# Kernel optimization log

Hardware: AMD Instinct MI355X
Metric: run time of the kernel (lower is better)

## Reference

```python
import jax, jax.numpy as jnp
import numpy as np

B, T, C = 4, 2048, 1024
NH, HS = 16, 64            # n_head, head_size
BL, SL = 32, 16            # block_length, stride_length


def setup_inputs() -> dict:
    key = jax.random.key(0)
    ks = jax.random.split(key, 7)
    def lin(k, shape, fan_in):
        return jax.random.normal(k, shape, jnp.float32) * (1.0 / np.sqrt(fan_in))
    return {
        "x": jax.random.normal(ks[0], (B, T, C), jnp.float32),
        "W_attn": lin(ks[1], (3 * C, C), C),          # c_attn weight (bias=False)
        "W_proj": lin(ks[2], (C, C), C),              # c_proj weight
        "pos_emb": jax.random.normal(ks[3], (T, HS), jnp.float32) * 0.02,
        "W_fc": lin(ks[4], (4 * HS, BL * HS), BL * HS),   # compression c_fc
        "W_cproj": lin(ks[5], (HS, 4 * HS), 4 * HS),      # compression c_proj
        "ln_w": jnp.ones((HS,), jnp.float32),             # compression LayerNorm (bias=False)
    }


def _compress(h, pos_emb, W_fc, W_cproj, ln_w):
    # h: [B, nh, T, hs] -> [B, nh, num_blocks, hs] ; sliding windows of len BL, stride SL
    Bb, nh, Tt, hs = h.shape
    nb = max(1, (Tt - BL) // SL + 1)
    idx = jnp.arange(nb)[:, None] * SL + jnp.arange(BL)[None, :]        # [nb, BL]
    blocks = h[:, :, idx, :] + pos_emb[:BL][None, None, None, :, :]     # [B,nh,nb,BL,hs]
    flat = blocks.reshape(Bb, nh, nb, BL * hs)
    z = jax.nn.gelu(jnp.einsum('bnkf,gf->bnkg', flat, W_fc), approximate=False)
    z = jnp.einsum('bnkg,hg->bnkh', z, W_cproj)
    mu = jnp.mean(z, axis=-1, keepdims=True)
    var = jnp.var(z, axis=-1, keepdims=True)
    return (z - mu) / jnp.sqrt(var + 1e-5) * ln_w


def reference(x, W_attn, W_proj, pos_emb, W_fc, W_cproj, ln_w):
    Bb, Tt, Cc = x.shape
    qkv = x @ W_attn.T                                   # [B,T,3C]
    q, k, v = jnp.split(qkv, 3, axis=-1)
    q = q.reshape(Bb, Tt, NH, HS).transpose(0, 2, 1, 3)  # [B,nh,T,hs]
    k = k.reshape(Bb, Tt, NH, HS).transpose(0, 2, 1, 3)
    v = v.reshape(Bb, Tt, NH, HS).transpose(0, 2, 1, 3)

    # Computed (and discarded) exactly as in the torch forward.
    _kc = _compress(k, pos_emb, W_fc, W_cproj, ln_w)
    _vc = _compress(v, pos_emb, W_fc, W_cproj, ln_w)

    # Flash branch: is_causal=True -> attn_mask=None -> plain causal SDPA
    scale = 1.0 / np.sqrt(HS)
    scores = jnp.einsum('bhqd,bhkd->bhqk', q, k) * scale          # [B,nh,T,T]
    causal = jnp.tril(jnp.ones((Tt, Tt), dtype=bool))
    scores = jnp.where(causal, scores, -jnp.inf)
    att = jax.nn.softmax(scores, axis=-1)
    y = jnp.einsum('bhqk,bhkd->bhqd', att, v)                     # [B,nh,T,hs]
    y = y.transpose(0, 2, 1, 3).reshape(Bb, Tt, Cc)
    return y @ W_proj.T
```

## Files before the change

kernel.cpp:

```cpp
#include <hip/hip_runtime.h>
#include <hip/hip_bf16.h>
#include <stdint.h>


typedef __bf16 bf16x8 __attribute__((ext_vector_type(8)));
typedef float f32x4 __attribute__((ext_vector_type(4)));
typedef __hip_bfloat16 bf16;

#define B_ 4
#define T_ 2048
#define C_ 1024
#define NH_ 16
#define HS_ 64
#define NEG_BIG (-30000.0f)
#define SCALE_LOG2E 0.180336880111f

__device__ __forceinline__ bool detect_fp32(const unsigned short* px) {
  const int lane = threadIdx.x & 63;
  const unsigned short u = px[2 * lane];
  const int e = (u >> 7) & 0xff;
  const bool plausible = (e >= 117) && (e <= 137);
  return __popcll(__ballot(plausible)) < 32;
}

__device__ __forceinline__ void load_lds16(const bf16* g, bf16* l) {
  __builtin_amdgcn_global_load_lds(
      (const __attribute__((address_space(1))) void*)(uintptr_t)g,
      (__attribute__((address_space(3))) void*)(uintptr_t)l, 16, 0, 0);
}

__device__ __forceinline__ uint4 ld8f(const void* base, size_t elt) {
  const float* fp = (const float*)base + elt;
  float4 f0 = *(const float4*)(fp);
  float4 f1 = *(const float4*)(fp + 4);
  union { bf16 h[8]; uint4 u; } r;
  r.h[0] = __float2bfloat16(f0.x); r.h[1] = __float2bfloat16(f0.y);
  r.h[2] = __float2bfloat16(f0.z); r.h[3] = __float2bfloat16(f0.w);
  r.h[4] = __float2bfloat16(f1.x); r.h[5] = __float2bfloat16(f1.y);
  r.h[6] = __float2bfloat16(f1.z); r.h[7] = __float2bfloat16(f1.w);
  return r.u;
}

__global__ __launch_bounds__(256) void convert3(
    const void* __restrict__ x, const void* __restrict__ wa,
    const void* __restrict__ wp, bf16* __restrict__ xb, bf16* __restrict__ wab,
    bf16* __restrict__ wpb, const unsigned short* __restrict__ probe) {
  const bool f32 = detect_fp32(probe);
  int blk = blockIdx.x;
  const void* src;
  bf16* dst;
  if (blk < 4096) {
    src = x; dst = xb;
  } else if (blk < 4096 + 1536) {
    blk -= 4096; src = wa; dst = wab;
  } else {
    blk -= 4096 + 1536; src = wp; dst = wpb;
  }
  const size_t i = ((size_t)blk * 256 + threadIdx.x) * 8;
  if (f32)
    *(uint4*)(dst + i) = ld8f(src, i);
  else
    *(uint4*)(dst + i) = *(const uint4*)((const bf16*)src + i);
}

template <int IN_MODE, int OUT_MODE>
__global__ __launch_bounds__(256, 2) void gemm_bt(
    const void* __restrict__ A, const void* __restrict__ B, void* __restrict__ C,
    bf16* __restrict__ k_ws, bf16* __restrict__ v_ws,
    const unsigned short* __restrict__ in_probe,
    const unsigned short* __restrict__ out_probe, int M, int N, int K) {
  __shared__ bf16 As[2][128 * 32];
  __shared__ bf16 Bs[2][128 * 32];

  const bool f32b = in_probe ? detect_fp32(in_probe) : false;
  const bool f32a = (IN_MODE == 0) && f32b;
  const bool f32out =
      (OUT_MODE == 0) && (out_probe ? detect_fp32(out_probe) : false);

  const int tid = threadIdx.x;
  const int lane = tid & 63;
  const int wid = tid >> 6;
  const int quad = lane >> 4;
  const int col = lane & 15;
  const int m0 = blockIdx.y * 128;
  const int n0 = blockIdx.x * 128;
  const int wm = (wid >> 1) * 64;
  const int wn = (wid & 1) * 64;
  const bool vsec = (OUT_MODE == 1) && ((n0 >> 10) == 2);

  const size_t arow = (size_t)(m0 + (tid >> 2));
  const size_t brow = (size_t)(n0 + (tid >> 2));
  const int chunk = (tid & 3) * 8;
  const size_t astep = (IN_MODE == 0) ? (size_t)64 * K : (size_t)64 * HS_;

  f32x4 acc[4][4] = {};

  auto a_ptr = [&](int k0) -> const bf16* {
    if (IN_MODE == 0) return (const bf16*)A + arow * K + chunk + k0;
    const int b = m0 >> 11;
    const int tloc = (m0 & 2047) + (tid >> 2);
    return (const bf16*)A +
           ((((size_t)b * NH_) + (k0 >> 6)) * T_ + tloc) * HS_ + (k0 & 32) +
           chunk;
  };

  if (f32a) {
    uint4 a0 = ld8f(A, arow * K + chunk);
    uint4 a1 = ld8f(A, (arow + 64) * K + chunk);
    *(uint4*)(&As[0][0] + tid * 8) = a0;
    *(uint4*)(&As[0][0] + 2048 + tid * 8) = a1;
  } else {
    const bf16* ap = a_ptr(0);
    load_lds16(ap, &As[0][0] + tid * 8);
    load_lds16(ap + astep, &As[0][0] + 2048 + tid * 8);
  }
  if (f32b) {
    uint4 b0 = ld8f(B, brow * K + chunk);
    uint4 b1 = ld8f(B, (brow + 64) * K + chunk);
    *(uint4*)(&Bs[0][0] + tid * 8) = b0;
    *(uint4*)(&Bs[0][0] + 2048 + tid * 8) = b1;
  } else {
    load_lds16((const bf16*)B + brow * K + chunk, &Bs[0][0] + tid * 8);
    load_lds16((const bf16*)B + (brow + 64) * K + chunk,
               &Bs[0][0] + 2048 + tid * 8);
  }
  __syncthreads();

  int cur = 0;
  for (int k0 = 0; k0 < K; k0 += 32) {
    const int kn = k0 + 32;
    const bool hasn = kn < K;
    const int nxt = cur ^ 1;

    uint4 a0, a1, b0, b1;
    bool wra = false, wrb = false;
    if (hasn) {
      if (f32a) {
        a0 = ld8f(A, arow * K + chunk + kn);
        a1 = ld8f(A, (arow + 64) * K + chunk + kn);
        wra = true;
      } else {
        const bf16* ap = a_ptr(kn);
        load_lds16(ap, &As[nxt][0] + tid * 8);
        load_lds16(ap + astep, &As[nxt][0] + 2048 + tid * 8);
      }
      if (f32b) {
        b0 = ld8f(B, brow * K + chunk + kn);
        b1 = ld8f(B, (brow + 64) * K + chunk + kn);
        wrb = true;
      } else {
        load_lds16((const bf16*)B + brow * K + chunk + kn,
                   &Bs[nxt][0] + tid * 8);
        load_lds16((const bf16*)B + (brow + 64) * K + chunk + kn,
                   &Bs[nxt][0] + 2048 + tid * 8);
      }
    }

    bf16x8 af[4], bfr[4];
#pragma unroll
    for (int t = 0; t < 4; ++t) {
      af[t] = *(const bf16x8*)(&As[cur][0] + (wm + t * 16 + col) * 32 + quad * 8);
      bfr[t] = *(const bf16x8*)(&Bs[cur][0] + (wn + t * 16 + col) * 32 + quad * 8);
    }
    if (vsec) {
#pragma unroll
      for (int tm = 0; tm < 4; ++tm)
#pragma unroll
        for (int tn = 0; tn < 4; ++tn)
          acc[tm][tn] = __builtin_amdgcn_mfma_f32_16x16x32_bf16(
              bfr[tn], af[tm], acc[tm][tn], 0, 0, 0);
    } else {
#pragma unroll
      for (int tm = 0; tm < 4; ++tm)
#pragma unroll
        for (int tn = 0; tn < 4; ++tn)
          acc[tm][tn] = __builtin_amdgcn_mfma_f32_16x16x32_bf16(
              af[tm], bfr[tn], acc[tm][tn], 0, 0, 0);
    }

    if (wra) {
      *(uint4*)(&As[nxt][0] + tid * 8) = a0;
      *(uint4*)(&As[nxt][0] + 2048 + tid * 8) = a1;
    }
    if (wrb) {
      *(uint4*)(&Bs[nxt][0] + tid * 8) = b0;
      *(uint4*)(&Bs[nxt][0] + 2048 + tid * 8) = b1;
    }
    __syncthreads();
    cur = nxt;
  }

  if (OUT_MODE == 0) {
#pragma unroll
    for (int tm = 0; tm < 4; ++tm) {
      const int mrow = m0 + wm + tm * 16 + quad * 4;
#pragma unroll
      for (int tn = 0; tn < 4; ++tn) {
        const int ncol = n0 + wn + tn * 16 + col;
#pragma unroll
        for (int r = 0; r < 4; ++r) {
          if (f32out)
            ((float*)C)[(size_t)(mrow + r) * N + ncol] = acc[tm][tn][r];
          else
            ((bf16*)C)[(size_t)(mrow + r) * N + ncol] =
                __float2bfloat16(acc[tm][tn][r]);
        }
      }
    }
  } else if (vsec) {
    const int b = m0 >> 11;
#pragma unroll
    for (int tm = 0; tm < 4; ++tm) {
      const int tloc = (m0 & 2047) + wm + tm * 16 + col;
#pragma unroll
      for (int tn = 0; tn < 4; ++tn) {
        const int vch = (n0 & (C_ - 1)) + wn + tn * 16 + quad * 4;
#pragma unroll
        for (int r = 0; r < 4; ++r) {
          const int h = (vch + r) >> 6, d = (vch + r) & 63;
          v_ws[(((size_t)b * NH_ + h) * HS_ + d) * T_ + tloc] =
              __float2bfloat16(acc[tm][tn][r]);
        }
      }
    }
  } else {
    const int sect = n0 >> 10;
    bf16* dst = (sect == 0) ? (bf16*)C : k_ws;
#pragma unroll
    for (int tm = 0; tm < 4; ++tm) {
      const int mrow = m0 + wm + tm * 16 + quad * 4;
#pragma unroll
      for (int tn = 0; tn < 4; ++tn) {
        const int c = (n0 + wn + tn * 16 + col) & (C_ - 1);
        const int h = c >> 6, d = c & 63;
#pragma unroll
        for (int r = 0; r < 4; ++r) {
          const int t = (mrow + r) & (T_ - 1);
          const int b = (mrow + r) >> 11;
          dst[(((size_t)b * NH_ + h) * T_ + t) * HS_ + d] =
              __float2bfloat16(acc[tm][tn][r]);
        }
      }
    }
  }
}

template <int SPLIT>
__global__ __launch_bounds__(256, 2) void attn(
    bf16* qy, const bf16* __restrict__ kws, const bf16* __restrict__ vws,
    float* __restrict__ po, float* __restrict__ pl) {
  __shared__ bf16 Ks[64 * 72];
  __shared__ bf16 Vs[64 * 72];
  __shared__ bf16 Ps[4][32 * 72];

  const int tid = threadIdx.x;
  const int lane = tid & 63;
  const int w = tid >> 6;
  const int quad = lane >> 4;
  const int col = lane & 15;
  const int x = (int)blockIdx.x;

  int qb, ck;
  if (SPLIT) {
    const unsigned long long lo = 0xC4D5E6F7FEDCBA98ULL;
    const unsigned int hi = 0xB3A29180u;
    const unsigned int cmask = 0x00AAAA00u;
    qb = (x < 16) ? (int)((lo >> (4 * x)) & 15)
                  : (int)((hi >> (4 * (x - 16))) & 15);
    ck = (int)((cmask >> x) & 1);
  } else {
    const int gx = (int)gridDim.x;
    const int hx = gx >> 1;
    qb = (x < hx) ? (gx - 1 - x) : (x - hx);
    ck = 0;
  }

  const int bh = blockIdx.y;
  const size_t head_off = (size_t)bh * T_ * HS_;

  const int ntall = 2 * (qb + 1);
  const int kt0 = SPLIT ? ck * 16 : 0;
  const int ntiles = SPLIT ? min(ntall - kt0, 16) : ntall;

  const int qrow = qb * 128 + w * 32 + col;
  const bf16* qp = qy + head_off + (size_t)qrow * HS_ + quad * 8;
  bf16x8 qf0a = *(const bf16x8*)(qp);
  bf16x8 qf1a = *(const bf16x8*)(qp + 32);
  bf16x8 qf0b = *(const bf16x8*)(qp + 16 * HS_);
  bf16x8 qf1b = *(const bf16x8*)(qp + 16 * HS_ + 32);
#pragma unroll
  for (int j = 0; j < 8; ++j) {
    qf0a[j] = (__bf16)((float)qf0a[j] * SCALE_LOG2E);
    qf1a[j] = (__bf16)((float)qf1a[j] * SCALE_LOG2E);
    qf0b[j] = (__bf16)((float)qf0b[j] * SCALE_LOG2E);
    qf1b[j] = (__bf16)((float)qf1b[j] * SCALE_LOG2E);
  }

  bf16x8 onesf;
#pragma unroll
  for (int j = 0; j < 8; ++j) onesf[j] = (__bf16)1.0f;

  f32x4 oa[4] = {}, ob[4] = {};
  f32x4 lacca = {}, laccb = {};

  bf16* pw = &Ps[w][0];

  const int srow = tid >> 3, sch = tid & 7;
  const bf16* kg = kws + head_off + (size_t)(kt0 * 64 + srow) * HS_ + sch * 8;
  const bf16* vg = vws + ((size_t)bh * HS_ + srow) * T_ + kt0 * 64 + sch * 8;
  bf16* kl0 = Ks + srow * 72 + sch * 8;
  bf16* kl1 = Ks + (srow + 32) * 72 + sch * 8;
  bf16* vl0 = Vs + srow * 72 + sch * 8;
  bf16* vl1 = Vs + (srow + 32) * 72 + sch * 8;

  uint4 kr0 = *(const uint4*)(kg);
  uint4 kr1 = *(const uint4*)(kg + (size_t)32 * HS_);
  uint4 vr0 = *(const uint4*)(vg);
  uint4 vr1 = *(const uint4*)(vg + (size_t)32 * T_);

  const int qga = qb * 128 + w * 32 + col;
  const int diag_start = 2 * qb;

  for (int kt = 0; kt < ntiles; ++kt) {
    const int ktg = kt0 + kt;
    const int k0 = ktg * 64;
    __syncthreads();
    *(uint4*)kl0 = kr0;
    *(uint4*)kl1 = kr1;
    *(uint4*)vl0 = vr0;
    *(uint4*)vl1 = vr1;
    __syncthreads();
    if (kt + 1 < ntiles) {
      kg += (size_t)64 * HS_;
      vg += 64;
      kr0 = *(const uint4*)(kg);
      kr1 = *(const uint4*)(kg + (size_t)32 * HS_);
      vr0 = *(const uint4*)(vg);
      vr1 = *(const uint4*)(vg + (size_t)32 * T_);
    }

    f32x4 sa[4], sb[4];
#pragma unroll
    for (int nt = 0; nt < 4; ++nt) {
      const bf16* kp = Ks + (nt * 16 + col) * 72 + quad * 8;
      bf16x8 kf0 = *(const bf16x8*)(kp);
      bf16x8 kf1 = *(const bf16x8*)(kp + 32);
      f32x4 a = {-32.0f, -32.0f, -32.0f, -32.0f};
      a = __builtin_amdgcn_mfma_f32_16x16x32_bf16(kf0, qf0a, a, 0, 0, 0);
      a = __builtin_amdgcn_mfma_f32_16x16x32_bf16(kf1, qf1a, a, 0, 0, 0);
      sa[nt] = a;
      f32x4 b = {-32.0f, -32.0f, -32.0f, -32.0f};
      b = __builtin_amdgcn_mfma_f32_16x16x32_bf16(kf0, qf0b, b, 0, 0, 0);
      b = __builtin_amdgcn_mfma_f32_16x16x32_bf16(kf1, qf1b, b, 0, 0, 0);
      sb[nt] = b;
    }

    if (ktg >= diag_start) {
#pragma unroll
      for (int nt = 0; nt < 4; ++nt) {
        const int key = k0 + nt * 16 + quad * 4;
#pragma unroll
        for (int r = 0; r < 4; ++r) {
          if (key + r > qga) sa[nt][r] = NEG_BIG;
          if (key + r > qga + 16) sb[nt][r] = NEG_BIG;
        }
      }
    }

#pragma unroll
    for (int nt = 0; nt < 4; ++nt) {
      union { ushort u[4]; uint2 v; } pa, pb;
#pragma unroll
      for (int r = 0; r < 4; ++r) {
        pa.u[r] = __bfloat16_as_ushort(__float2bfloat16(exp2f(sa[nt][r])));
        pb.u[r] = __bfloat16_as_ushort(__float2bfloat16(exp2f(sb[nt][r])));
      }
      *(uint2*)(pw + col * 72 + nt * 16 + quad * 4) = pa.v;
      *(uint2*)(pw + (col + 16) * 72 + nt * 16 + quad * 4) = pb.v;
    }

    __asm__ __volatile__("s_waitcnt lgkmcnt(0)" ::: "memory");

#pragma unroll
    for (int half = 0; half < 2; ++half) {
      bf16x8 pfa = *(const bf16x8*)(pw + col * 72 + half * 32 + quad * 8);
      bf16x8 pfb = *(const bf16x8*)(pw + (col + 16) * 72 + half * 32 + quad * 8);
      lacca = __builtin_amdgcn_mfma_f32_16x16x32_bf16(pfa, onesf, lacca, 0, 0, 0);
      laccb = __builtin_amdgcn_mfma_f32_16x16x32_bf16(pfb, onesf, laccb, 0, 0, 0);
#pragma unroll
      for (int dt = 0; dt < 4; ++dt) {
        bf16x8 vf = *(const bf16x8*)(Vs + (dt * 16 + col) * 72 + half * 32 +
                                     quad * 8);
        oa[dt] = __builtin_amdgcn_mfma_f32_16x16x32_bf16(pfa, vf, oa[dt], 0, 0, 0);
        ob[dt] = __builtin_amdgcn_mfma_f32_16x16x32_bf16(pfb, vf, ob[dt], 0, 0, 0);
      }
    }
  }

  const bool dosplit = SPLIT && (qb >= 8);
  if (!dosplit) {
    float inva[4], invb[4];
#pragma unroll
    for (int r = 0; r < 4; ++r) {
      inva[r] = 1.0f / lacca[r];
      invb[r] = 1.0f / laccb[r];
    }
#pragma unroll
    for (int dt = 0; dt < 4; ++dt)
#pragma unroll
      for (int r = 0; r < 4; ++r) {
        const int qa = qb * 128 + w * 32 + quad * 4 + r;
        qy[head_off + (size_t)qa * HS_ + dt * 16 + col] =
            __float2bfloat16(oa[dt][r] * inva[r]);
        qy[head_off + (size_t)(qa + 16) * HS_ + dt * 16 + col] =
            __float2bfloat16(ob[dt][r] * invb[r]);
      }
  } else {
    const int slot = ((qb - 8) * 64 + bh) * 2 + ck;
    float* o = po + (size_t)slot * (128 * 64);
#pragma unroll
    for (int dt = 0; dt < 4; ++dt)
#pragma unroll
      for (int r = 0; r < 4; ++r) {
        const int qa = w * 32 + quad * 4 + r;
        o[(size_t)qa * 64 + dt * 16 + col] = oa[dt][r];
        o[(size_t)(qa + 16) * 64 + dt * 16 + col] = ob[dt][r];
      }
    if (col == 0) {
      float* lp = pl + (size_t)slot * 128;
#pragma unroll
      for (int r = 0; r < 4; ++r) {
        lp[w * 32 + quad * 4 + r] = lacca[r];
        lp[w * 32 + 16 + quad * 4 + r] = laccb[r];
      }
    }
  }
}

__global__ __launch_bounds__(256) void attn_combine(
    bf16* __restrict__ qy, const float* __restrict__ po,
    const float* __restrict__ pl) {
  const int qb = 8 + (int)blockIdx.x;
  const int bh = (int)blockIdx.y;
  const int pair = ((qb - 8) * 64 + bh) * 2;
  const float* o0 = po + (size_t)pair * (128 * 64);
  const float* o1 = o0 + 128 * 64;
  const float* l0 = pl + (size_t)pair * 128;
  const float* l1 = l0 + 128;
  const int q = threadIdx.x >> 1;
  const int d0 = (threadIdx.x & 1) * 32;
  const float inv = 1.0f / (l0[q] + l1[q]);
  const size_t base =
      (size_t)bh * T_ * HS_ + (size_t)(qb * 128 + q) * HS_ + d0;
  const size_t ob = (size_t)q * 64 + d0;
#pragma unroll
  for (int j0 = 0; j0 < 32; j0 += 8) {
    union { bf16 h[8]; uint4 u; } out;
#pragma unroll
    for (int j = 0; j < 8; ++j)
      out.h[j] = __float2bfloat16((o0[ob + j0 + j] + o1[ob + j0 + j]) * inv);
    *(uint4*)(qy + base + j0) = out.u;
  }
}

extern "C" void kernel_launch(void* const* d_in, const int* in_sizes, int n_in,
                              void* d_out, int out_size, void* d_ws, size_t ws_size,
                              hipStream_t stream) {
  const void* x = d_in[0];
  const void* W_attn = d_in[1];
  const void* W_proj = d_in[2];
  const unsigned short* probe = (const unsigned short*)d_in[0];

  const size_t qkv_elems = (size_t)B_ * NH_ * T_ * HS_;
  const size_t xe = (size_t)B_ * T_ * C_;
  const size_t wae = (size_t)3 * C_ * C_;
  const size_t wpe = (size_t)C_ * C_;

  bf16* q_ws = (bf16*)d_ws;
  bf16* k_ws = q_ws + qkv_elems;
  bf16* v_ws = k_ws + qkv_elems;
  bf16* x_bf = v_ws + qkv_elems;
  bf16* wa_bf = x_bf + xe;
  bf16* wp_bf = wa_bf + wae;
  const size_t need = (3 * qkv_elems + xe + wae + wpe) * sizeof(bf16);

  float* po = (float*)(wp_bf + wpe);
  float* pl = po + (size_t)1024 * 128 * 64;
  const size_t need2 =
      need + ((size_t)1024 * 128 * 64 + (size_t)1024 * 128) * sizeof(float);

  const int M = B_ * T_;

  if (ws_size >= need) {
    convert3<<<6144, 256, 0, stream>>>(x, W_attn, W_proj, x_bf, wa_bf, wp_bf,
                                       probe);
    gemm_bt<0, 1><<<dim3(3 * C_ / 128, M / 128), 256, 0, stream>>>(
        x_bf, wa_bf, q_ws, k_ws, v_ws, nullptr, nullptr, M, 3 * C_, C_);
    if (ws_size >= need2) {
      attn<1><<<dim3(24, B_ * NH_), 256, 0, stream>>>(q_ws, k_ws, v_ws, po, pl);
      attn_combine<<<dim3(8, B_ * NH_), 256, 0, stream>>>(q_ws, po, pl);
    } else {
      attn<0><<<dim3(T_ / 128, B_ * NH_), 256, 0, stream>>>(q_ws, k_ws, v_ws,
                                                            nullptr, nullptr);
    }
    gemm_bt<1, 0><<<dim3(C_ / 128, M / 128), 256, 0, stream>>>(
        q_ws, wp_bf, d_out, nullptr, nullptr, nullptr, probe, M, C_, C_);
  } else {
    gemm_bt<0, 1><<<dim3(3 * C_ / 128, M / 128), 256, 0, stream>>>(
        x, W_attn, q_ws, k_ws, v_ws, probe, nullptr, M, 3 * C_, C_);
    attn<0><<<dim3(T_ / 128, B_ * NH_), 256, 0, stream>>>(q_ws, k_ws, v_ws,
                                                          nullptr, nullptr);
    gemm_bt<1, 0><<<dim3(C_ / 128, M / 128), 256, 0, stream>>>(
        q_ws, W_proj, d_out, nullptr, nullptr, probe, probe, M, C_, C_);
  }
}
```

Measured before the change: 285.2 us.

## Add 256x256-tile 8-wave QKV GEMM with async LDS pipelining

Replaces the 128x128 QKV projection GEMM with a new 512-thread kernel that uses 256x256 tiles, double-buffered direct-to-LDS loads with XOR-swizzled layout, interleaved half-tile staging, and priority-raised MFMA phases. It also swizzles the block order for L2 locality and swaps the MFMA operands for the V section so V can be written transposed. The aim is higher arithmetic intensity and better overlap of loads with MFMA in the largest GEMM. The trade-off is much more register and LDS pressure, and a fragile hand-written waitcnt and barrier schedule.

```diff
diff --git a/kernel.cpp b/kernel.cpp
--- a/kernel.cpp
+++ b/kernel.cpp
@@ -61,6 +61,199 @@
     *(uint4*)(dst + i) = ld8f(src, i);
   else
     *(uint4*)(dst + i) = *(const uint4*)((const bf16*)src + i);
+}
+
+__global__ __launch_bounds__(512, 2) void gemm8_qkv(
+    const bf16* __restrict__ A, const bf16* __restrict__ Bm,
+    bf16* __restrict__ q_ws, bf16* __restrict__ k_ws,
+    bf16* __restrict__ v_ws) {
+  __shared__ bf16 Asm[2][2][256][32];
+  __shared__ bf16 Bsm[2][2][256][32];
+
+  const int tid = threadIdx.x;
+  const int lane = tid & 63;
+  const int wid = tid >> 6;
+  const int wr = wid >> 2;
+  const int wc = wid & 3;
+  const int quad = lane >> 4;
+  const int col = lane & 15;
+
+  const int flat = (int)blockIdx.y * 12 + (int)blockIdx.x;
+  const int swz = (flat & 7) * 48 + (flat >> 3);
+  const int n0 = (swz % 12) * 256;
+  const int m0 = (swz / 12) * 256;
+  const bool vsec = (n0 >> 10) == 2;
+
+  constexpr int NT = 1024 / 64;
+
+  const int c0 = tid, c1 = 512 + tid;
+  const int r0 = c0 >> 2, s0 = (c0 & 3) ^ ((r0 >> 1) & 3);
+  const int r1 = c1 >> 2, s1 = (c1 & 3) ^ ((r1 >> 1) & 3);
+  const size_t ga0 = (size_t)(m0 + r0) * 1024 + s0 * 8;
+  const size_t ga1 = (size_t)(m0 + r1) * 1024 + s1 * 8;
+  const size_t gb0 = (size_t)(n0 + r0) * 1024 + s0 * 8;
+  const size_t gb1 = (size_t)(n0 + r1) * 1024 + s1 * 8;
+
+  auto stageA = [&](int T, int h) {
+    bf16* base = &Asm[T & 1][h][0][0];
+    const int kk = T * 64 + h * 32;
+    load_lds16(A + ga0 + kk, base + c0 * 8);
+    load_lds16(A + ga1 + kk, base + c1 * 8);
+  };
+  auto stageB = [&](int T, int h) {
+    bf16* base = &Bsm[T & 1][h][0][0];
+    const int kk = T * 64 + h * 32;
+    load_lds16(Bm + gb0 + kk, base + c0 * 8);
+    load_lds16(Bm + gb1 + kk, base + c1 * 8);
+  };
+
+  const int aq = quad ^ ((col >> 1) & 3);
+
+  f32x4 acc[8][4] = {};
+  bf16x8 pA[8];
+
+  stageA(0, 0); stageB(0, 0); stageA(0, 1); stageB(0, 1);
+  stageA(1, 0); stageB(1, 0); stageA(1, 1);
+  asm volatile("s_waitcnt vmcnt(6)" ::: "memory");
+  __builtin_amdgcn_s_barrier();
+
+  for (int t = 0; t < NT; ++t) {
+    const bf16* Ab = (const bf16*)Asm + (t & 1) * 16384;
+    const bf16* Bb = (const bf16*)Bsm + (t & 1) * 16384;
+
+#pragma unroll
+    for (int m = 0; m < 8; ++m)
+      pA[m] = *(const bf16x8*)(Ab + (wr * 128 + m * 16 + col) * 32 + aq * 8);
+    bf16x8 b0 = *(const bf16x8*)(Bb + (wc * 64 + 0 + col) * 32 + aq * 8);
+    bf16x8 b1 = *(const bf16x8*)(Bb + (wc * 64 + 16 + col) * 32 + aq * 8);
+    if (t + 1 < NT) stageB(t + 1, 1);
+    __builtin_amdgcn_s_barrier();
+    asm volatile("s_waitcnt lgkmcnt(0)" ::: "memory");
+    __builtin_amdgcn_s_setprio(1);
+    if (vsec) {
+#pragma unroll
+      for (int m = 0; m < 8; ++m) {
+        acc[m][0] = __builtin_amdgcn_mfma_f32_16x16x32_bf16(b0, pA[m], acc[m][0], 0, 0, 0);
+        acc[m][1] = __builtin_amdgcn_mfma_f32_16x16x32_bf16(b1, pA[m], acc[m][1], 0, 0, 0);
+      }
+    } else {
+#pragma unroll
+      for (int m = 0; m < 8; ++m) {
+        acc[m][0] = __builtin_amdgcn_mfma_f32_16x16x32_bf16(pA[m], b0, acc[m][0], 0, 0, 0);
+        acc[m][1] = __builtin_amdgcn_mfma_f32_16x16x32_bf16(pA[m], b1, acc[m][1], 0, 0, 0);
+      }
+    }
+    __builtin_amdgcn_s_setprio(0);
+    __builtin_amdgcn_s_barrier();
+
+    bf16x8 b2 = *(const bf16x8*)(Bb + (wc * 64 + 32 + col) * 32 + aq * 8);
+    bf16x8 b3 = *(const bf16x8*)(Bb + (wc * 64 + 48 + col) * 32 + aq * 8);
+    if (t + 2 < NT) stageA(t + 2, 0);
+    __builtin_amdgcn_s_barrier();
+    asm volatile("s_waitcnt lgkmcnt(0)" ::: "memory");
+    __builtin_amdgcn_s_setprio(1);
+    if (vsec) {
+#pragma unroll
+      for (int m = 0; m < 8; ++m) {
+        acc[m][2] = __builtin_amdgcn_mfma_f32_16x16x32_bf16(b2, pA[m], acc[m][2], 0, 0, 0);
+        acc[m][3] = __builtin_amdgcn_mfma_f32_16x16x32_bf16(b3, pA[m], acc[m][3], 0, 0, 0);
+      }
+    } else {
+#pragma unroll
+      for (int m = 0; m < 8; ++m) {
+        acc[m][2] = __builtin_amdgcn_mfma_f32_16x16x32_bf16(pA[m], b2, acc[m][2], 0, 0, 0);
+        acc[m][3] = __builtin_amdgcn_mfma_f32_16x16x32_bf16(pA[m], b3, acc[m][3], 0, 0, 0);
+      }
+    }
+    __builtin_amdgcn_s_setprio(0);
+    __builtin_amdgcn_s_barrier();
+
+    Ab += 8192;
+    Bb += 8192;
+#pragma unroll
+    for (int m = 0; m < 8; ++m)
+      pA[m] = *(const bf16x8*)(Ab + (wr * 128 + m * 16 + col) * 32 + aq * 8);
+    b0 = *(const bf16x8*)(Bb + (wc * 64 + 0 + col) * 32 + aq * 8);
+    b1 = *(const bf16x8*)(Bb + (wc * 64 + 16 + col) * 32 + aq * 8);
+    if (t + 2 < NT) stageB(t + 2, 0);
+    __builtin_amdgcn_s_barrier();
+    asm volatile("s_waitcnt lgkmcnt(0)" ::: "memory");
+    __builtin_amdgcn_s_setprio(1);
+    if (vsec) {
+#pragma unroll
+      for (int m = 0; m < 8; ++m) {
+        acc[m][0] = __builtin_amdgcn_mfma_f32_16x16x32_bf16(b0, pA[m], acc[m][0], 0, 0, 0);
+        acc[m][1] = __builtin_amdgcn_mfma_f32_16x16x32_bf16(b1, pA[m], acc[m][1], 0, 0, 0);
+      }
+    } else {
+#pragma unroll
+      for (int m = 0; m < 8; ++m) {
+        acc[m][0] = __builtin_amdgcn_mfma_f32_16x16x32_bf16(pA[m], b0, acc[m][0], 0, 0, 0);
+        acc[m][1] = __builtin_amdgcn_mfma_f32_16x16x32_bf16(pA[m], b1, acc[m][1], 0, 0, 0);
+      }
+    }
+    __builtin_amdgcn_s_setprio(0);
+    __builtin_amdgcn_s_barrier();
+
+    b2 = *(const bf16x8*)(Bb + (wc * 64 + 32 + col) * 32 + aq * 8);
+    b3 = *(const bf16x8*)(Bb + (wc * 64 + 48 + col) * 32 + aq * 8);
+    if (t + 2 < NT) stageA(t + 2, 1);
+    __builtin_amdgcn_s_barrier();
+    asm volatile("s_waitcnt lgkmcnt(0)" ::: "memory");
+    __builtin_amdgcn_s_setprio(1);
+    if (vsec) {
+#pragma unroll
+      for (int m = 0; m < 8; ++m) {
+        acc[m][2] = __builtin_amdgcn_mfma_f32_16x16x32_bf16(b2, pA[m], acc[m][2], 0, 0, 0);
+        acc[m][3] = __builtin_amdgcn_mfma_f32_16x16x32_bf16(b3, pA[m], acc[m][3], 0, 0, 0);
+      }
+    } else {
+#pragma unroll
+      for (int m = 0; m < 8; ++m) {
+        acc[m][2] = __builtin_amdgcn_mfma_f32_16x16x32_bf16(pA[m], b2, acc[m][2], 0, 0, 0);
+        acc[m][3] = __builtin_amdgcn_mfma_f32_16x16x32_bf16(pA[m], b3, acc[m][3], 0, 0, 0);
+      }
+    }
+    __builtin_amdgcn_s_setprio(0);
+    if (t + 2 < NT)
+      asm volatile("s_waitcnt vmcnt(6)" ::: "memory");
+    else
+      asm volatile("s_waitcnt vmcnt(0)" ::: "memory");
+    __builtin_amdgcn_s_barrier();
+  }
+
+  const int b = m0 >> 11;
+  if (!vsec) {
+    bf16* dst = ((n0 >> 10) == 0) ? q_ws : k_ws;
+#pragma unroll
+    for (int m = 0; m < 8; ++m) {
+      const int mrow = (m0 & 2047) + wr * 128 + m * 16 + quad * 4;
+#pragma unroll
+      for (int n = 0; n < 4; ++n) {
+        const int cc = (n0 & 1023) + wc * 64 + n * 16 + col;
+        const int h = cc >> 6, d = cc & 63;
+#pragma unroll
+        for (int r = 0; r < 4; ++r)
+          dst[(((size_t)b * NH_ + h) * T_ + mrow + r) * HS_ + d] =
+              __float2bfloat16(acc[m][n][r]);
+      }
+    }
+  } else {
+#pragma unroll
+    for (int m = 0; m < 8; ++m) {
+      const int tloc = (m0 & 2047) + wr * 128 + m * 16 + col;
+#pragma unroll
+      for (int n = 0; n < 4; ++n) {
+        const int vch = (n0 & 1023) + wc * 64 + n * 16 + quad * 4;
+#pragma unroll
+        for (int r = 0; r < 4; ++r) {
+          const int h = (vch + r) >> 6, d = (vch + r) & 63;
+          v_ws[(((size_t)b * NH_ + h) * HS_ + d) * T_ + tloc] =
+              __float2bfloat16(acc[m][n][r]);
+        }
+      }
+    }
+  }
 }
 
 template <int IN_MODE, int OUT_MODE>
@@ -494,8 +687,7 @@
   if (ws_size >= need) {
     convert3<<<6144, 256, 0, stream>>>(x, W_attn, W_proj, x_bf, wa_bf, wp_bf,
                                        probe);
-    gemm_bt<0, 1><<<dim3(3 * C_ / 128, M / 128), 256, 0, stream>>>(
-        x_bf, wa_bf, q_ws, k_ws, v_ws, nullptr, nullptr, M, 3 * C_, C_);
+    gemm8_qkv<<<dim3(12, 32), 512, 0, stream>>>(x_bf, wa_bf, q_ws, k_ws, v_ws);
     if (ws_size >= need2) {
       attn<1><<<dim3(24, B_ * NH_), 256, 0, stream>>>(q_ws, k_ws, v_ws, po, pl);
       attn_combine<<<dim3(8, B_ * NH_), 256, 0, stream>>>(q_ws, po, pl);
```

Measured after the change: 512.1 us. 79.6% more time.
